# Kernel optimization log

Measured on AMD Instinct MI355X. Metric: run time of the kernel, lower is better.

## Reference

```python
import jax, jax.numpy as jnp
import numpy as np

N = 50000
E = 800000
IN_F, HID, OUT_F = 512, 256, 64
BN_EPS = 1e-5


def setup_inputs() -> dict:
    key = jax.random.key(0)
    ks = jax.random.split(key, 8)
    x = jax.random.normal(ks[0], (N, IN_F), dtype=jnp.float32)
    edge_rows = jax.random.randint(ks[1], (E,), 0, N, dtype=jnp.int32)
    edge_cols = jax.random.randint(ks[2], (E,), 0, N, dtype=jnp.int32)
    edge_vals = jax.random.uniform(ks[3], (E,), dtype=jnp.float32)
    # xavier_uniform for weights, zeros for biases (as in the torch module)
    lim1 = float(np.sqrt(6.0 / (IN_F + HID)))
    lim2 = float(np.sqrt(6.0 / (HID + OUT_F)))
    W1 = jax.random.uniform(ks[4], (IN_F, HID), minval=-lim1, maxval=lim1, dtype=jnp.float32)
    b1 = jnp.zeros((HID,), dtype=jnp.float32)
    W2 = jax.random.uniform(ks[5], (HID, OUT_F), minval=-lim2, maxval=lim2, dtype=jnp.float32)
    b2 = jnp.zeros((OUT_F,), dtype=jnp.float32)
    # BatchNorm affine params (torch defaults: weight=1, bias=0)
    gamma1 = jnp.ones((HID,), dtype=jnp.float32)
    beta1 = jnp.zeros((HID,), dtype=jnp.float32)
    gamma2 = jnp.ones((OUT_F,), dtype=jnp.float32)
    beta2 = jnp.zeros((OUT_F,), dtype=jnp.float32)
    return dict(x=x, edge_rows=edge_rows, edge_cols=edge_cols, edge_vals=edge_vals,
                W1=W1, b1=b1, gamma1=gamma1, beta1=beta1,
                W2=W2, b2=b2, gamma2=gamma2, beta2=beta2)


def _spmm(rows, cols, vals, dense):
    # sparse [N,N] @ dense [N,F] via gather + segment-sum scatter
    msgs = vals[:, None] * dense[cols]            # [E, F]
    return jax.ops.segment_sum(msgs, rows, num_segments=N)


def _batchnorm(h, gamma, beta):
    # training-mode BatchNorm1d: batch statistics over nodes (biased var)
    mean = jnp.mean(h, axis=0)
    var = jnp.var(h, axis=0)
    return gamma * (h - mean) * jax.lax.rsqrt(var + BN_EPS) + beta


def reference(x, edge_rows, edge_cols, edge_vals,
              W1, b1, gamma1, beta1, W2, b2, gamma2, beta2):
    # layer 1: GCN conv -> BN -> ReLU (dropout is identity in eval / reference)
    h = _spmm(edge_rows, edge_cols, edge_vals, x @ W1) + b1
    h = jax.nn.relu(_batchnorm(h, gamma1, beta1))
    # layer 2: GCN conv -> BN -> log_softmax over classes
    h = _spmm(edge_rows, edge_cols, edge_vals, h @ W2) + b2
    h = _batchnorm(h, gamma2, beta2)
    return jax.nn.log_softmax(h, axis=1)
```

## Files before the change

### kernel.cpp

```cpp
#include <hip/hip_runtime.h>

typedef __attribute__((ext_vector_type(8))) short short8;
typedef __attribute__((ext_vector_type(4))) float f32x4;
typedef __attribute__((ext_vector_type(8))) unsigned short ushort8;

__device__ __forceinline__ unsigned short f2bf(float f) {
  unsigned int u = __builtin_bit_cast(unsigned int, f);
  u += 0x7fffu + ((u >> 16) & 1u);
  return (unsigned short)(u >> 16);
}
__device__ __forceinline__ float bf2f(unsigned short b) {
  return __builtin_bit_cast(float, ((unsigned int)b) << 16);
}
__device__ __forceinline__ void gload_lds16(const void* g, void* l) {
  __builtin_amdgcn_global_load_lds(
      (const __attribute__((address_space(1))) void*)g,
      (__attribute__((address_space(3))) void*)l, 16, 0, 0);
}

__global__ __launch_bounds__(256) void cvt_weights(
    const float* __restrict__ W1, const float* __restrict__ W2,
    unsigned short* __restrict__ w1t, unsigned short* __restrict__ w2t)
{
  int idx = blockIdx.x * 256 + threadIdx.x;
  if (idx < 131072) {
    int n = idx >> 9, k = idx & 511;
    w1t[idx] = f2bf(W1[(size_t)k * 256 + n]);
  } else if (idx < 131072 + 16384) {
    int i = idx - 131072;
    int n = i >> 8, k = i & 255;
    w2t[i] = f2bf(W2[(size_t)k * 64 + n]);
  }
}

__global__ __launch_bounds__(256) void gemm1_mfma(
    const float* __restrict__ x,
    const unsigned short* __restrict__ w1t,
    unsigned short* __restrict__ H1,
    int M)
{
  __shared__ unsigned short As[2][64 * 32];
  __shared__ unsigned short Bs[2][256 * 32];
  const int tid = threadIdx.x;
  const int wid = tid >> 6, lane = tid & 63;
  const int wc = wid;
  const int m0 = blockIdx.x * 64;

  const int ar = tid >> 2;
  const int ac = tid & 3;
  const int arow = m0 + ar;
  const int aphys = ac ^ ((ar >> 1) & 3);

  const int bq = lane >> 2;
  const int bslotx = (lane & 3) ^ ((lane >> 3) & 3);

  float4 alo, ahi;
  auto loadA = [&](int k0) {
    alo = make_float4(0.f, 0.f, 0.f, 0.f); ahi = alo;
    if (arow < M) {
      alo = *(const float4*)&x[(size_t)arow * 512 + k0 + ac * 8];
      ahi = *(const float4*)&x[(size_t)arow * 512 + k0 + ac * 8 + 4];
    }
  };
  auto writeA = [&](int buf) {
    ushort8 o;
    o[0] = f2bf(alo.x); o[1] = f2bf(alo.y); o[2] = f2bf(alo.z); o[3] = f2bf(alo.w);
    o[4] = f2bf(ahi.x); o[5] = f2bf(ahi.y); o[6] = f2bf(ahi.z); o[7] = f2bf(ahi.w);
    *(ushort8*)((char*)As[buf] + ar * 64 + aphys * 16) = o;
  };
  auto stageB = [&](int k0, int buf) {
#pragma unroll
    for (int i = 0; i < 4; ++i) {
      int g = wid + 4 * i;
      int col = g * 16 + bq;
      gload_lds16(&w1t[(size_t)col * 512 + k0 + bslotx * 8],
                  (char*)Bs[buf] + g * 1024);
    }
  };

  f32x4 acc[4][4] = {};

  loadA(0);
  stageB(0, 0);
  writeA(0);
  __syncthreads();

  for (int kt = 0; kt < 16; ++kt) {
    const int cur = kt & 1, nxt = cur ^ 1;
    if (kt < 15) {
      loadA((kt + 1) * 32);
      stageB((kt + 1) * 32, nxt);
    }
    short8 a[4], b[4];
#pragma unroll
    for (int m = 0; m < 4; ++m) {
      int row = m * 16 + (lane & 15);
      int phys = (lane >> 4) ^ ((row >> 1) & 3);
      a[m] = *(const short8*)((const char*)As[cur] + row * 64 + phys * 16);
    }
#pragma unroll
    for (int n = 0; n < 4; ++n) {
      int col = wc * 64 + n * 16 + (lane & 15);
      int phys = (lane >> 4) ^ ((col >> 1) & 3);
      b[n] = *(const short8*)((const char*)Bs[cur] + col * 64 + phys * 16);
    }
#pragma unroll
    for (int m = 0; m < 4; ++m)
#pragma unroll
      for (int n = 0; n < 4; ++n)
        acc[m][n] = __builtin_amdgcn_mfma_f32_16x16x32_bf16(a[m], b[n], acc[m][n], 0, 0, 0);
    if (kt < 15) writeA(nxt);
    __syncthreads();
  }

  const int colbase = wc * 64 + (lane & 15);
#pragma unroll
  for (int m = 0; m < 4; ++m) {
    int rowbase = m0 + m * 16 + (lane >> 4) * 4;
#pragma unroll
    for (int j = 0; j < 4; ++j) {
      int row = rowbase + j;
      if (row < M) {
#pragma unroll
        for (int n = 0; n < 4; ++n)
          H1[(size_t)row * 256 + colbase + n * 16] = f2bf(acc[m][n][j]);
      }
    }
  }
}

__global__ __launch_bounds__(256) void gemm2_mfma(
    const unsigned short* __restrict__ A,
    const unsigned short* __restrict__ w2t,
    const float* __restrict__ scsh,
    unsigned short* __restrict__ H2,
    int M)
{
  __shared__ unsigned short As[128 * 64];
  __shared__ unsigned short Bs[64 * 64];
  const int tid = threadIdx.x;
  const int wid = tid >> 6, lane = tid & 63;
  const int wr = wid >> 1, wc = wid & 1;
  const int m0 = blockIdx.x * 128;

  const int srow = tid >> 3;
  const int ls = ((tid & 7) ^ (srow & 7)) * 8;
  const unsigned short* gB = &w2t[(size_t)srow * 256 + ls];
  char* lB = (char*)Bs + (size_t)wid * 1024;

  f32x4 acc[4][2] = {};

  for (int kt = 0; kt < 4; ++kt) {
    const int k0 = kt * 64;
#pragma unroll
    for (int i = 0; i < 2; ++i)
      gload_lds16(gB + (size_t)i * 32 * 256 + k0, lB + (size_t)i * 4096);
#pragma unroll
    for (int i = 0; i < 4; ++i) {
      int chunk = tid + 256 * i;
      int r = chunk >> 3, c = chunk & 7;
      int gk = k0 + c * 8;
      ushort8 u = *(const ushort8*)&A[(size_t)(m0 + r) * 256 + gk];
      float4 sc0 = *(const float4*)&scsh[gk];
      float4 sc1 = *(const float4*)&scsh[gk + 4];
      float4 sh0 = *(const float4*)&scsh[256 + gk];
      float4 sh1 = *(const float4*)&scsh[256 + gk + 4];
      ushort8 o;
      o[0] = f2bf(fmaxf(bf2f(u[0]) * sc0.x + sh0.x, 0.f));
      o[1] = f2bf(fmaxf(bf2f(u[1]) * sc0.y + sh0.y, 0.f));
      o[2] = f2bf(fmaxf(bf2f(u[2]) * sc0.z + sh0.z, 0.f));
      o[3] = f2bf(fmaxf(bf2f(u[3]) * sc0.w + sh0.w, 0.f));
      o[4] = f2bf(fmaxf(bf2f(u[4]) * sc1.x + sh1.x, 0.f));
      o[5] = f2bf(fmaxf(bf2f(u[5]) * sc1.y + sh1.y, 0.f));
      o[6] = f2bf(fmaxf(bf2f(u[6]) * sc1.z + sh1.z, 0.f));
      o[7] = f2bf(fmaxf(bf2f(u[7]) * sc1.w + sh1.w, 0.f));
      *(ushort8*)((char*)As + r * 128 + ((c ^ (r & 7)) * 16)) = o;
    }
    __syncthreads();

#pragma unroll
    for (int kk = 0; kk < 2; ++kk) {
      short8 a[4], b[2];
#pragma unroll
      for (int m = 0; m < 4; ++m) {
        int row = wr * 64 + m * 16 + (lane & 15);
        int phys = (kk * 4 + (lane >> 4)) ^ (row & 7);
        a[m] = *(const short8*)((const char*)As + row * 128 + phys * 16);
      }
#pragma unroll
      for (int n = 0; n < 2; ++n) {
        int col = wc * 32 + n * 16 + (lane & 15);
        int phys = (kk * 4 + (lane >> 4)) ^ (col & 7);
        b[n] = *(const short8*)((const char*)Bs + col * 128 + phys * 16);
      }
#pragma unroll
      for (int m = 0; m < 4; ++m)
#pragma unroll
        for (int n = 0; n < 2; ++n)
          acc[m][n] = __builtin_amdgcn_mfma_f32_16x16x32_bf16(a[m], b[n], acc[m][n], 0, 0, 0);
    }
    __syncthreads();
  }

  const int colbase = wc * 32 + (lane & 15);
#pragma unroll
  for (int m = 0; m < 4; ++m) {
    int rowbase = m0 + wr * 64 + m * 16 + (lane >> 4) * 4;
#pragma unroll
    for (int j = 0; j < 4; ++j) {
      int row = rowbase + j;
      if (row < M) {
#pragma unroll
        for (int n = 0; n < 2; ++n)
          H2[(size_t)row * 64 + colbase + n * 16] = f2bf(acc[m][n][j]);
      }
    }
  }
}

__global__ __launch_bounds__(256) void edge_hist(
    const int* __restrict__ rows, int* __restrict__ cnt, int E)
{
  int e = blockIdx.x * 256 + threadIdx.x;
  if (e < E) atomicAdd(&cnt[rows[e]], 1);
}

__global__ __launch_bounds__(256) void scan_blocksum(
    const int* __restrict__ cnt, int* __restrict__ bsum, int Nrows)
{
  int i = blockIdx.x * 256 + threadIdx.x;
  int v = (i < Nrows) ? cnt[i] : 0;
#pragma unroll
  for (int off = 1; off < 64; off <<= 1) v += __shfl_xor(v, off);
  __shared__ int wsum[4];
  if ((threadIdx.x & 63) == 0) wsum[threadIdx.x >> 6] = v;
  __syncthreads();
  if (threadIdx.x == 0)
    bsum[blockIdx.x] = wsum[0] + wsum[1] + wsum[2] + wsum[3];
}

__global__ __launch_bounds__(256) void scan_boff(
    const int* __restrict__ bsum, int* __restrict__ boff, int NB)
{
  __shared__ int lds[256];
  int t = threadIdx.x;
  int v = (t < NB) ? bsum[t] : 0;
  lds[t] = v;
  __syncthreads();
  for (int off = 1; off < 256; off <<= 1) {
    int u = (t >= off) ? lds[t - off] : 0;
    __syncthreads();
    lds[t] += u;
    __syncthreads();
  }
  boff[t] = (t == 0) ? 0 : lds[t - 1];
}

__global__ __launch_bounds__(256) void scan_write(
    const int* __restrict__ cnt, const int* __restrict__ boff,
    int* __restrict__ rowptr, int* __restrict__ cursor, int Nrows, int E)
{
  __shared__ int lds[256];
  int t = threadIdx.x;
  int i = blockIdx.x * 256 + t;
  int v = (i < Nrows) ? cnt[i] : 0;
  lds[t] = v;
  __syncthreads();
  for (int off = 1; off < 256; off <<= 1) {
    int u = (t >= off) ? lds[t - off] : 0;
    __syncthreads();
    lds[t] += u;
    __syncthreads();
  }
  int excl = boff[blockIdx.x] + lds[t] - v;
  if (i < Nrows) { rowptr[i] = excl; cursor[i] = excl; }
  if (i == Nrows) rowptr[i] = E;
}

__global__ __launch_bounds__(256) void edge_scatter(
    const int* __restrict__ rows, const int* __restrict__ cols,
    const float* __restrict__ vals, int* __restrict__ cursor,
    int2* __restrict__ spack, int E)
{
  int e = blockIdx.x * 256 + threadIdx.x;
  if (e < E) {
    int r = rows[e];
    int p = atomicAdd(&cursor[r], 1);
    spack[p] = make_int2(cols[e], __float_as_int(vals[e]));
  }
}

__global__ __launch_bounds__(256) void spmm_gather_bf(
    const int* __restrict__ rowptr, const int2* __restrict__ sp,
    const unsigned short* __restrict__ D,
    unsigned short* __restrict__ out, int Nrows)
{
  const int lane = threadIdx.x & 63;
  const int r = blockIdx.x * 4 + (threadIdx.x >> 6);
  if (r >= Nrows) return;
  const int s = rowptr[r], e = rowptr[r + 1];
  float4 acc0 = make_float4(0.f, 0.f, 0.f, 0.f);
  float4 acc1 = make_float4(0.f, 0.f, 0.f, 0.f);
  int j = s;
  for (; j + 7 < e; j += 8) {
    int2 p[8];
    ushort4 d[8];
#pragma unroll
    for (int t = 0; t < 8; ++t) p[t] = sp[j + t];
#pragma unroll
    for (int t = 0; t < 8; ++t)
      d[t] = *(const ushort4*)&D[(size_t)p[t].x * 256 + lane * 4];
#pragma unroll
    for (int t = 0; t < 8; t += 2) {
      float v0 = __int_as_float(p[t].y), v1 = __int_as_float(p[t + 1].y);
      acc0.x = fmaf(v0, bf2f(d[t].x), acc0.x); acc0.y = fmaf(v0, bf2f(d[t].y), acc0.y);
      acc0.z = fmaf(v0, bf2f(d[t].z), acc0.z); acc0.w = fmaf(v0, bf2f(d[t].w), acc0.w);
      acc1.x = fmaf(v1, bf2f(d[t + 1].x), acc1.x); acc1.y = fmaf(v1, bf2f(d[t + 1].y), acc1.y);
      acc1.z = fmaf(v1, bf2f(d[t + 1].z), acc1.z); acc1.w = fmaf(v1, bf2f(d[t + 1].w), acc1.w);
    }
  }
  for (; j + 1 < e; j += 2) {
    int2 p0 = sp[j], p1 = sp[j + 1];
    ushort4 d0 = *(const ushort4*)&D[(size_t)p0.x * 256 + lane * 4];
    ushort4 d1 = *(const ushort4*)&D[(size_t)p1.x * 256 + lane * 4];
    float v0 = __int_as_float(p0.y), v1 = __int_as_float(p1.y);
    acc0.x = fmaf(v0, bf2f(d0.x), acc0.x); acc0.y = fmaf(v0, bf2f(d0.y), acc0.y);
    acc0.z = fmaf(v0, bf2f(d0.z), acc0.z); acc0.w = fmaf(v0, bf2f(d0.w), acc0.w);
    acc1.x = fmaf(v1, bf2f(d1.x), acc1.x); acc1.y = fmaf(v1, bf2f(d1.y), acc1.y);
    acc1.z = fmaf(v1, bf2f(d1.z), acc1.z); acc1.w = fmaf(v1, bf2f(d1.w), acc1.w);
  }
  if (j < e) {
    int2 p = sp[j];
    float v = __int_as_float(p.y);
    ushort4 d = *(const ushort4*)&D[(size_t)p.x * 256 + lane * 4];
    acc0.x = fmaf(v, bf2f(d.x), acc0.x); acc0.y = fmaf(v, bf2f(d.y), acc0.y);
    acc0.z = fmaf(v, bf2f(d.z), acc0.z); acc0.w = fmaf(v, bf2f(d.w), acc0.w);
  }
  ushort4 ov;
  ov.x = f2bf(acc0.x + acc1.x); ov.y = f2bf(acc0.y + acc1.y);
  ov.z = f2bf(acc0.z + acc1.z); ov.w = f2bf(acc0.w + acc1.w);
  *(ushort4*)&out[(size_t)r * 256 + lane * 4] = ov;
}

__global__ __launch_bounds__(256) void spmm_gather_bf64(
    const int* __restrict__ rowptr, const int2* __restrict__ sp,
    const unsigned short* __restrict__ D,
    float* __restrict__ out, int Nrows)
{
  const int lane = threadIdx.x & 63;
  const int r = blockIdx.x * 4 + (threadIdx.x >> 6);
  if (r >= Nrows) return;
  const int s = rowptr[r], e = rowptr[r + 1];
  float acc0 = 0.f, acc1 = 0.f;
  int j = s;
  for (; j + 7 < e; j += 8) {
    int2 p[8];
    float d[8];
#pragma unroll
    for (int t = 0; t < 8; ++t) p[t] = sp[j + t];
#pragma unroll
    for (int t = 0; t < 8; ++t) d[t] = bf2f(D[(size_t)p[t].x * 64 + lane]);
#pragma unroll
    for (int t = 0; t < 8; t += 2) {
      acc0 = fmaf(__int_as_float(p[t].y), d[t], acc0);
      acc1 = fmaf(__int_as_float(p[t + 1].y), d[t + 1], acc1);
    }
  }
  for (; j < e; ++j) {
    int2 p = sp[j];
    acc0 = fmaf(__int_as_float(p.y), bf2f(D[(size_t)p.x * 64 + lane]), acc0);
  }
  out[(size_t)r * 64 + lane] = acc0 + acc1;
}

__global__ __launch_bounds__(256) void bn_stats_bf256(
    const unsigned short* __restrict__ H, float* __restrict__ partials, int Nrows)
{
  const int cc = threadIdx.x & 31;
  const int c = cc * 8;
  const int rr = threadIdx.x >> 5;
  float s[8] = {}, q[8] = {};
  for (int r = blockIdx.x * 8 + rr; r < Nrows; r += gridDim.x * 8) {
    ushort8 u = *(const ushort8*)&H[(size_t)r * 256 + c];
#pragma unroll
    for (int j = 0; j < 8; ++j) {
      float f = bf2f(u[j]);
      s[j] += f; q[j] += f * f;
    }
  }
  __shared__ float lds[256][16];
  float* L = lds[threadIdx.x];
#pragma unroll
  for (int j = 0; j < 8; ++j) { L[j] = s[j]; L[8 + j] = q[j]; }
  __syncthreads();
  if (rr == 0) {
#pragma unroll
    for (int r2 = 1; r2 < 8; ++r2) {
      float* Mm = lds[cc + r2 * 32];
#pragma unroll
      for (int j = 0; j < 8; ++j) { s[j] += Mm[j]; q[j] += Mm[8 + j]; }
    }
    float* P = &partials[(size_t)blockIdx.x * 512];
#pragma unroll
    for (int j = 0; j < 8; ++j) { P[c + j] = s[j]; P[256 + c + j] = q[j]; }
  }
}

__global__ __launch_bounds__(256) void bn_stats64(
    const float* __restrict__ H, float* __restrict__ partials, int Nrows)
{
  const int cc = threadIdx.x % 16;
  const int c = cc * 4;
  const int rr = threadIdx.x / 16;
  float4 s = make_float4(0.f, 0.f, 0.f, 0.f);
  float4 q = make_float4(0.f, 0.f, 0.f, 0.f);
  for (int r = blockIdx.x * 16 + rr; r < Nrows; r += gridDim.x * 16) {
    float4 v = *(const float4*)&H[(size_t)r * 64 + c];
    s.x += v.x; s.y += v.y; s.z += v.z; s.w += v.w;
    q.x += v.x * v.x; q.y += v.y * v.y; q.z += v.z * v.z; q.w += v.w * v.w;
  }
  __shared__ float lds[256][8];
  float* L = lds[threadIdx.x];
  L[0] = s.x; L[1] = s.y; L[2] = s.z; L[3] = s.w;
  L[4] = q.x; L[5] = q.y; L[6] = q.z; L[7] = q.w;
  __syncthreads();
  if (rr == 0) {
#pragma unroll
    for (int r2 = 1; r2 < 16; ++r2) {
      float* Mm = lds[cc + r2 * 16];
      s.x += Mm[0]; s.y += Mm[1]; s.z += Mm[2]; s.w += Mm[3];
      q.x += Mm[4]; q.y += Mm[5]; q.z += Mm[6]; q.w += Mm[7];
    }
    float* P = &partials[(size_t)blockIdx.x * 128];
    *(float4*)&P[c] = s;
    *(float4*)&P[64 + c] = q;
  }
}

template<int C>
__global__ __launch_bounds__(256) void bn_finalize_par(
    const float* __restrict__ partials,
    const float* __restrict__ gamma, const float* __restrict__ beta,
    float* __restrict__ scsh, int G, float invN)
{
  const int c = blockIdx.x;
  const int t = threadIdx.x;
  float sum = 0.f, sq = 0.f;
  for (int g = t; g < G; g += 256) {
    sum += partials[(size_t)g * 2 * C + c];
    sq  += partials[(size_t)g * 2 * C + C + c];
  }
#pragma unroll
  for (int off = 1; off < 64; off <<= 1) {
    sum += __shfl_xor(sum, off);
    sq  += __shfl_xor(sq, off);
  }
  __shared__ float ws[4][2];
  if ((t & 63) == 0) { ws[t >> 6][0] = sum; ws[t >> 6][1] = sq; }
  __syncthreads();
  if (t == 0) {
    sum = ws[0][0] + ws[1][0] + ws[2][0] + ws[3][0];
    sq  = ws[0][1] + ws[1][1] + ws[2][1] + ws[3][1];
    float mean = sum * invN;
    float var = sq * invN - mean * mean;
    float rstd = rsqrtf(var + 1e-5f);
    float sc = gamma[c] * rstd;
    scsh[c] = sc;
    scsh[C + c] = beta[c] - mean * sc;
  }
}

__global__ __launch_bounds__(256) void bn_lsm(
    const float* __restrict__ H, const float* __restrict__ scsh,
    float* __restrict__ out, int Nrows)
{
  int lane = threadIdx.x & 63;
  int r = blockIdx.x * 4 + (threadIdx.x >> 6);
  if (r >= Nrows) return;
  float y = H[(size_t)r * 64 + lane] * scsh[lane] + scsh[64 + lane];
  float m = y;
#pragma unroll
  for (int off = 32; off >= 1; off >>= 1) m = fmaxf(m, __shfl_xor(m, off));
  float ex = expf(y - m);
  float s = ex;
#pragma unroll
  for (int off = 32; off >= 1; off >>= 1) s += __shfl_xor(s, off);
  out[(size_t)r * 64 + lane] = (y - m) - logf(s);
}

extern "C" void kernel_launch(void* const* d_in, const int* in_sizes, int n_in,
                              void* d_out, int out_size, void* d_ws, size_t ws_size,
                              hipStream_t stream) {
  const float* x      = (const float*)d_in[0];
  const int*   erow   = (const int*)  d_in[1];
  const int*   ecol   = (const int*)  d_in[2];
  const float* eval   = (const float*)d_in[3];
  const float* W1     = (const float*)d_in[4];
  const float* gamma1 = (const float*)d_in[6];
  const float* beta1  = (const float*)d_in[7];
  const float* W2     = (const float*)d_in[8];
  const float* gamma2 = (const float*)d_in[10];
  const float* beta2  = (const float*)d_in[11];

  const int N = in_sizes[0] / 512;
  const int E = in_sizes[1];

  char* ws = (char*)d_ws;
  unsigned short* H1b   = (unsigned short*)(ws + 0);
  float* partials1      = (float*)(ws + 0);
  unsigned short* H2b   = (unsigned short*)(ws + 0);
  float* H2AGG          = (float*)(ws + 12800000);
  unsigned short* H1AGGb= (unsigned short*)(ws + 51200000);
  float* partials2      = (float*)(ws + 51200000);
  unsigned short* w1t   = (unsigned short*)(ws + 76865536);
  float* scsh1          = (float*)(ws + 77127680);
  float* scsh2          = (float*)(ws + 77129728);
  int*   rowptr         = (int*)(ws + 77130240);
  int*   cnt            = (int*)(ws + 77330244);
  int*   cursor         = (int*)(ws + 77530244);
  int2*  spack          = (int2*)(ws + 77730248);
  int*   bsum           = (int*)(ws + 84130248);
  int*   boff           = (int*)(ws + 84131272);
  unsigned short* w2t   = (unsigned short*)(ws + 84132352);

  hipMemsetAsync(cnt, 0, (size_t)N * 4, stream);

  const dim3 blk(256);
  const int eblocks = (E + 255) / 256;
  const int NB = (N + 255) / 256;

  edge_hist<<<eblocks, blk, 0, stream>>>(erow, cnt, E);
  scan_blocksum<<<NB, blk, 0, stream>>>(cnt, bsum, N);
  scan_boff<<<1, blk, 0, stream>>>(bsum, boff, NB);
  scan_write<<<NB + 1, blk, 0, stream>>>(cnt, boff, rowptr, cursor, N, E);
  edge_scatter<<<eblocks, blk, 0, stream>>>(erow, ecol, eval, cursor, spack, E);

  cvt_weights<<<576, blk, 0, stream>>>(W1, W2, w1t, w2t);

  gemm1_mfma<<<(N + 63) / 64, blk, 0, stream>>>(x, w1t, H1b, N);
  spmm_gather_bf<<<(N + 3) / 4, blk, 0, stream>>>(rowptr, spack, H1b, H1AGGb, N);
  bn_stats_bf256<<<256, blk, 0, stream>>>(H1AGGb, partials1, N);
  bn_finalize_par<256><<<256, blk, 0, stream>>>(partials1, gamma1, beta1, scsh1, 256, 1.0f / N);
  gemm2_mfma<<<(N + 127) / 128, blk, 0, stream>>>(H1AGGb, w2t, scsh1, H2b, N);
  spmm_gather_bf64<<<(N + 3) / 4, blk, 0, stream>>>(rowptr, spack, H2b, H2AGG, N);
  bn_stats64<<<256, blk, 0, stream>>>(H2AGG, partials2, N);
  bn_finalize_par<64><<<64, blk, 0, stream>>>(partials2, gamma2, beta2, scsh2, 256, 1.0f / N);
  bn_lsm<<<(N + 3) / 4, blk, 0, stream>>>(H2AGG, scsh2, (float*)d_out, N);
}
```

Measured before the change: 273.8 us.

## Split gemm1 into N-halves with XCD-aware block mapping; software-pipeline SpMM gathers

```diff
diff --git a/kernel.cpp b/kernel.cpp
--- a/kernel.cpp
+++ b/kernel.cpp
@@ -40,15 +40,23 @@
     int M)
 {
   __shared__ unsigned short As[2][64 * 32];
-  __shared__ unsigned short Bs[2][256 * 32];
+  __shared__ unsigned short Bs[2][128 * 32];
   const int tid = threadIdx.x;
   const int wid = tid >> 6, lane = tid & 63;
-  const int wc = wid;
-  const int m0 = blockIdx.x * 64;
+
+  const int mstripes = (M + 63) >> 6;
+  const int cpx = (mstripes + 7) >> 3;
+  const int k8 = blockIdx.x & 7;
+  const int s  = blockIdx.x >> 3;
+  const int mstripe = k8 * cpx + (s >> 1);
+  const int nh = s & 1;
+  if (mstripe >= mstripes) return;
+  const int m0 = mstripe * 64;
+  const int n0 = nh * 128;
 
   const int ar = tid >> 2;
   const int ac = tid & 3;
-  const int arow = m0 + ar;
+  const int arow = min(m0 + ar, M - 1);
   const int aphys = ac ^ ((ar >> 1) & 3);
 
   const int bq = lane >> 2;
@@ -56,11 +64,8 @@
 
   float4 alo, ahi;
   auto loadA = [&](int k0) {
-    alo = make_float4(0.f, 0.f, 0.f, 0.f); ahi = alo;
-    if (arow < M) {
-      alo = *(const float4*)&x[(size_t)arow * 512 + k0 + ac * 8];
-      ahi = *(const float4*)&x[(size_t)arow * 512 + k0 + ac * 8 + 4];
-    }
+    alo = *(const float4*)&x[(size_t)arow * 512 + k0 + ac * 8];
+    ahi = *(const float4*)&x[(size_t)arow * 512 + k0 + ac * 8 + 4];
   };
   auto writeA = [&](int buf) {
     ushort8 o;
@@ -70,15 +75,15 @@
   };
   auto stageB = [&](int k0, int buf) {
 #pragma unroll
-    for (int i = 0; i < 4; ++i) {
+    for (int i = 0; i < 2; ++i) {
       int g = wid + 4 * i;
-      int col = g * 16 + bq;
+      int col = n0 + g * 16 + bq;
       gload_lds16(&w1t[(size_t)col * 512 + k0 + bslotx * 8],
                   (char*)Bs[buf] + g * 1024);
     }
   };
 
-  f32x4 acc[4][4] = {};
+  f32x4 acc[4][2] = {};
 
   loadA(0);
   stageB(0, 0);
@@ -91,7 +96,7 @@
       loadA((kt + 1) * 32);
       stageB((kt + 1) * 32, nxt);
     }
-    short8 a[4], b[4];
+    short8 a[4], b[2];
 #pragma unroll
     for (int m = 0; m < 4; ++m) {
       int row = m * 16 + (lane & 15);
@@ -99,21 +104,21 @@
       a[m] = *(const short8*)((const char*)As[cur] + row * 64 + phys * 16);
     }
 #pragma unroll
-    for (int n = 0; n < 4; ++n) {
-      int col = wc * 64 + n * 16 + (lane & 15);
-      int phys = (lane >> 4) ^ ((col >> 1) & 3);
-      b[n] = *(const short8*)((const char*)Bs[cur] + col * 64 + phys * 16);
+    for (int n = 0; n < 2; ++n) {
+      int lc = wid * 32 + n * 16 + (lane & 15);
+      int phys = (lane >> 4) ^ ((lc >> 1) & 3);
+      b[n] = *(const short8*)((const char*)Bs[cur] + lc * 64 + phys * 16);
     }
 #pragma unroll
     for (int m = 0; m < 4; ++m)
 #pragma unroll
-      for (int n = 0; n < 4; ++n)
+      for (int n = 0; n < 2; ++n)
         acc[m][n] = __builtin_amdgcn_mfma_f32_16x16x32_bf16(a[m], b[n], acc[m][n], 0, 0, 0);
     if (kt < 15) writeA(nxt);
     __syncthreads();
   }
 
-  const int colbase = wc * 64 + (lane & 15);
+  const int colbase = n0 + wid * 32 + (lane & 15);
 #pragma unroll
   for (int m = 0; m < 4; ++m) {
     int rowbase = m0 + m * 16 + (lane >> 4) * 4;
@@ -122,7 +127,7 @@
       int row = rowbase + j;
       if (row < M) {
 #pragma unroll
-        for (int n = 0; n < 4; ++n)
+        for (int n = 0; n < 2; ++n)
           H1[(size_t)row * 256 + colbase + n * 16] = f2bf(acc[m][n][j]);
       }
     }
@@ -302,14 +307,27 @@
   float4 acc0 = make_float4(0.f, 0.f, 0.f, 0.f);
   float4 acc1 = make_float4(0.f, 0.f, 0.f, 0.f);
   int j = s;
-  for (; j + 7 < e; j += 8) {
-    int2 p[8];
-    ushort4 d[8];
+  int2 p[8]; ushort4 d[8];
+  bool have = (j + 8 <= e);
+  if (have) {
 #pragma unroll
     for (int t = 0; t < 8; ++t) p[t] = sp[j + t];
 #pragma unroll
     for (int t = 0; t < 8; ++t)
       d[t] = *(const ushort4*)&D[(size_t)p[t].x * 256 + lane * 4];
+    j += 8;
+  }
+  while (have) {
+    int2 pn[8]; ushort4 dn[8];
+    const bool haven = (j + 8 <= e);
+    if (haven) {
+#pragma unroll
+      for (int t = 0; t < 8; ++t) pn[t] = sp[j + t];
+#pragma unroll
+      for (int t = 0; t < 8; ++t)
+        dn[t] = *(const ushort4*)&D[(size_t)pn[t].x * 256 + lane * 4];
+      j += 8;
+    }
 #pragma unroll
     for (int t = 0; t < 8; t += 2) {
       float v0 = __int_as_float(p[t].y), v1 = __int_as_float(p[t + 1].y);
@@ -318,6 +336,11 @@
       acc1.x = fmaf(v1, bf2f(d[t + 1].x), acc1.x); acc1.y = fmaf(v1, bf2f(d[t + 1].y), acc1.y);
       acc1.z = fmaf(v1, bf2f(d[t + 1].z), acc1.z); acc1.w = fmaf(v1, bf2f(d[t + 1].w), acc1.w);
     }
+    if (haven) {
+#pragma unroll
+      for (int t = 0; t < 8; ++t) { p[t] = pn[t]; d[t] = dn[t]; }
+    }
+    have = haven;
   }
   for (; j + 1 < e; j += 2) {
     int2 p0 = sp[j], p1 = sp[j + 1];
@@ -330,11 +353,11 @@
     acc1.z = fmaf(v1, bf2f(d1.z), acc1.z); acc1.w = fmaf(v1, bf2f(d1.w), acc1.w);
   }
   if (j < e) {
-    int2 p = sp[j];
-    float v = __int_as_float(p.y);
-    ushort4 d = *(const ushort4*)&D[(size_t)p.x * 256 + lane * 4];
-    acc0.x = fmaf(v, bf2f(d.x), acc0.x); acc0.y = fmaf(v, bf2f(d.y), acc0.y);
-    acc0.z = fmaf(v, bf2f(d.z), acc0.z); acc0.w = fmaf(v, bf2f(d.w), acc0.w);
+    int2 p0 = sp[j];
+    float v = __int_as_float(p0.y);
+    ushort4 d0 = *(const ushort4*)&D[(size_t)p0.x * 256 + lane * 4];
+    acc0.x = fmaf(v, bf2f(d0.x), acc0.x); acc0.y = fmaf(v, bf2f(d0.y), acc0.y);
+    acc0.z = fmaf(v, bf2f(d0.z), acc0.z); acc0.w = fmaf(v, bf2f(d0.w), acc0.w);
   }
   ushort4 ov;
   ov.x = f2bf(acc0.x + acc1.x); ov.y = f2bf(acc0.y + acc1.y);
@@ -353,22 +376,39 @@
   const int s = rowptr[r], e = rowptr[r + 1];
   float acc0 = 0.f, acc1 = 0.f;
   int j = s;
-  for (; j + 7 < e; j += 8) {
-    int2 p[8];
-    float d[8];
+  int2 p[8]; float d[8];
+  bool have = (j + 8 <= e);
+  if (have) {
 #pragma unroll
     for (int t = 0; t < 8; ++t) p[t] = sp[j + t];
 #pragma unroll
     for (int t = 0; t < 8; ++t) d[t] = bf2f(D[(size_t)p[t].x * 64 + lane]);
+    j += 8;
+  }
+  while (have) {
+    int2 pn[8]; float dn[8];
+    const bool haven = (j + 8 <= e);
+    if (haven) {
+#pragma unroll
+      for (int t = 0; t < 8; ++t) pn[t] = sp[j + t];
+#pragma unroll
+      for (int t = 0; t < 8; ++t) dn[t] = bf2f(D[(size_t)pn[t].x * 64 + lane]);
+      j += 8;
+    }
 #pragma unroll
     for (int t = 0; t < 8; t += 2) {
       acc0 = fmaf(__int_as_float(p[t].y), d[t], acc0);
       acc1 = fmaf(__int_as_float(p[t + 1].y), d[t + 1], acc1);
     }
+    if (haven) {
+#pragma unroll
+      for (int t = 0; t < 8; ++t) { p[t] = pn[t]; d[t] = dn[t]; }
+    }
+    have = haven;
   }
   for (; j < e; ++j) {
-    int2 p = sp[j];
-    acc0 = fmaf(__int_as_float(p.y), bf2f(D[(size_t)p.x * 64 + lane]), acc0);
+    int2 p0 = sp[j];
+    acc0 = fmaf(__int_as_float(p0.y), bf2f(D[(size_t)p0.x * 64 + lane]), acc0);
   }
   out[(size_t)r * 64 + lane] = acc0 + acc1;
 }
@@ -537,7 +577,9 @@
 
   cvt_weights<<<576, blk, 0, stream>>>(W1, W2, w1t, w2t);
 
-  gemm1_mfma<<<(N + 63) / 64, blk, 0, stream>>>(x, w1t, H1b, N);
+  const int mstripes = (N + 63) / 64;
+  const int cpx = (mstripes + 7) / 8;
+  gemm1_mfma<<<8 * cpx * 2, blk, 0, stream>>>(x, w1t, H1b, N);
   spmm_gather_bf<<<(N + 3) / 4, blk, 0, stream>>>(rowptr, spack, H1b, H1AGGb, N);
   bn_stats_bf256<<<256, blk, 0, stream>>>(H1AGGb, partials1, N);
   bn_finalize_par<256><<<256, blk, 0, stream>>>(partials1, gamma1, beta1, scsh1, 256, 1.0f / N);
```

After: 286.8 us. 1.05x slower.
